# Optimization experiments

Measured on AMD Instinct MI355X. Metric: run time of the kernel, lower is better.

Reference implementation:

```python
import jax, jax.numpy as jnp
import numpy as np

B, T, C = 2, 2048, 2048
H, KVH, HD = 16, 4, 128  # heads, kv heads, head_dim
G = H // KVH             # GQA group size
THETA = 10000.0


def _rope_cos_sin(t, hd, dtype):
    inv_freq = 1.0 / (THETA ** (jnp.arange(0, hd, 2, dtype=jnp.float32) / hd))
    pos = jnp.arange(t, dtype=jnp.float32)
    freqs = pos[:, None] * inv_freq[None, :]          # [T, hd/2]
    emb = jnp.concatenate([freqs, freqs], axis=-1)    # [T, hd]
    return jnp.cos(emb).astype(dtype), jnp.sin(emb).astype(dtype)


def _rotate_half(x):
    x1, x2 = jnp.split(x, 2, axis=-1)
    return jnp.concatenate([-x2, x1], axis=-1)


def setup_inputs() -> dict:
    key = jax.random.key(0)
    ks = jax.random.split(key, 5)
    s_in = 1.0 / np.sqrt(C)
    return {
        "x": jax.random.normal(ks[0], (B, T, C), jnp.float32),
        "wq": jax.random.normal(ks[1], (C, H * HD), jnp.float32) * s_in,
        "bq": jnp.zeros((H * HD,), jnp.float32),
        "wk": jax.random.normal(ks[2], (C, KVH * HD), jnp.float32) * s_in,
        "bk": jnp.zeros((KVH * HD,), jnp.float32),
        "wv": jax.random.normal(ks[3], (C, KVH * HD), jnp.float32) * s_in,
        "bv": jnp.zeros((KVH * HD,), jnp.float32),
        "wo": jax.random.normal(ks[4], (H * HD, C), jnp.float32) * (1.0 / np.sqrt(H * HD)),
    }


def reference(x, wq, bq, wk, bk, wv, bv, wo):
    b, t, c = x.shape
    q = (x @ wq + bq).reshape(b, t, H, HD).transpose(0, 2, 1, 3)    # [B,H,T,hd]
    k = (x @ wk + bk).reshape(b, t, KVH, HD).transpose(0, 2, 1, 3)  # [B,KVH,T,hd]
    v = (x @ wv + bv).reshape(b, t, KVH, HD).transpose(0, 2, 1, 3)

    cos, sin = _rope_cos_sin(t, HD, x.dtype)  # [T,hd]
    q = q * cos + _rotate_half(q) * sin
    k = k * cos + _rotate_half(k) * sin

    # GQA: group query heads over kv heads
    qg = q.reshape(b, KVH, G, t, HD)
    scale = 1.0 / np.sqrt(HD)
    scores = jnp.einsum('bkgtd,bksd->bkgts', qg, k) * scale  # [B,KVH,G,T,T]
    causal = jnp.tril(jnp.ones((t, t), bool))
    scores = jnp.where(causal, scores, jnp.finfo(scores.dtype).min)
    attn = jax.nn.softmax(scores, axis=-1)
    out = jnp.einsum('bkgts,bksd->bkgtd', attn, v)            # [B,KVH,G,T,hd]
    out = out.reshape(b, H, t, HD).transpose(0, 2, 1, 3).reshape(b, t, H * HD)
    return out @ wo
```

## Files before the change

### kernel.cpp

```cpp
#include <hip/hip_runtime.h>
#include <hip/hip_bf16.h>
#include <math.h>

#define B_ 2
#define T_ 2048
#define C_ 2048
#define H_ 16
#define KVH_ 4
#define HD_ 128
#define G_ (H_ / KVH_)
#define MROWS (B_ * T_)
#define NQKV (H_ * HD_ + 2 * KVH_ * HD_)
#define KOFF (H_ * HD_)
#define VOFF (H_ * HD_ + KVH_ * HD_)
#define L2T (13.287712379549449f / 64.0f)

typedef __hip_bfloat16 bf16;
typedef short bf16x8 __attribute__((ext_vector_type(8)));
typedef short bf16x4 __attribute__((ext_vector_type(4)));
typedef float f32x4 __attribute__((ext_vector_type(4)));

__device__ __forceinline__ void gload_lds16(const void* g, void* l) {
  __builtin_amdgcn_global_load_lds(
      (const __attribute__((address_space(1))) unsigned int*)g,
      (__attribute__((address_space(3))) unsigned int*)l, 16, 0, 0);
}

static __device__ __forceinline__ f32x4 mfma32k(bf16x8 a, bf16x8 b, f32x4 c) {
  return __builtin_amdgcn_mfma_f32_16x16x32_bf16(a, b, c, 0, 0, 0);
}

static __device__ __forceinline__ short f2bf(float x) {
  unsigned u = __builtin_bit_cast(unsigned, x);
  u += 0x7FFFu + ((u >> 16) & 1u);
  return (short)(u >> 16);
}

static __device__ __forceinline__ float bfh2f(short h) {
  unsigned u = ((unsigned)(unsigned short)h) << 16;
  return __builtin_bit_cast(float, u);
}

static __device__ __forceinline__ float fexp2(float x) {
#if __has_builtin(__builtin_amdgcn_exp2f)
  return __builtin_amdgcn_exp2f(x);
#else
  return exp2f(x);
#endif
}

__global__ __launch_bounds__(256) void prep_kernel(
    const float* __restrict__ x, bf16* __restrict__ xb,
    const float* __restrict__ wq, const float* __restrict__ wk,
    const float* __restrict__ wv, bf16* __restrict__ wqkvT,
    const float* __restrict__ wo, bf16* __restrict__ woT,
    float2* __restrict__ tab) {
  __shared__ float t[32][33];
  int bid = blockIdx.x;
  if (bid < 8192) {
    const int i = (bid * 256 + threadIdx.x) * 4;
    float4 v = *(const float4*)(x + i);
    xb[i + 0] = __float2bfloat16(v.x);
    xb[i + 1] = __float2bfloat16(v.y);
    xb[i + 2] = __float2bfloat16(v.z);
    xb[i + 3] = __float2bfloat16(v.w);
    return;
  }
  bid -= 8192;
  if (bid < 6144) {
    const int tx = threadIdx.x & 31, ty = threadIdx.x >> 5;
    const int c0 = (bid % 96) * 32;
    const int r0 = (bid / 96) * 32;
    const float* src;
    int nn, ld;
    if (c0 < KOFF)      { src = wq; nn = c0;        ld = 2048; }
    else if (c0 < VOFF) { src = wk; nn = c0 - KOFF; ld = 512; }
    else                { src = wv; nn = c0 - VOFF; ld = 512; }
#pragma unroll
    for (int it = 0; it < 4; ++it)
      t[ty + 8 * it][tx] = src[(size_t)(r0 + ty + 8 * it) * ld + nn + tx];
    __syncthreads();
#pragma unroll
    for (int it = 0; it < 4; ++it)
      wqkvT[(size_t)(c0 + ty + 8 * it) * 2048 + r0 + tx] =
          __float2bfloat16(t[tx][ty + 8 * it]);
    return;
  }
  bid -= 6144;
  if (bid < 4096) {
    const int tx = threadIdx.x & 31, ty = threadIdx.x >> 5;
    const int c0 = (bid & 63) * 32;
    const int r0 = (bid >> 6) * 32;
#pragma unroll
    for (int it = 0; it < 4; ++it)
      t[ty + 8 * it][tx] = wo[(size_t)(r0 + ty + 8 * it) * 2048 + c0 + tx];
    __syncthreads();
#pragma unroll
    for (int it = 0; it < 4; ++it)
      woT[(size_t)(c0 + ty + 8 * it) * 2048 + r0 + tx] =
          __float2bfloat16(t[tx][ty + 8 * it]);
    return;
  }
  bid -= 4096;
  {
    const int idx = bid * 256 + threadIdx.x;
    const int tt = idx >> 6, i = idx & 63;
    const float invf = fexp2(-(float)i * L2T);
    float s, c;
    __sincosf((float)tt * invf, &s, &c);
    tab[idx] = make_float2(c, s);
  }
}

__global__ __launch_bounds__(256) void pack_kv(const bf16* __restrict__ qkv,
                                               bf16* __restrict__ kp,
                                               bf16* __restrict__ vp,
                                               const float2* __restrict__ tab) {
  const int pid = blockIdx.x;
  if (pid < 512) {
    const int tile = pid & 63;
    const int bk = pid >> 6;
    const int b = bk >> 2, kvh = bk & 3;
#pragma unroll
    for (int u = 0; u < 2; ++u) {
      const int t = threadIdx.x + u * 256;
      const int kc = t >> 6, L = t & 63;
      const int trow = tile * 32 + ((L >> 2) & 3) * 8 + (kc >> 2) * 4 + (L & 3);
      const bf16* src = qkv + (size_t)(b * T_ + trow) * NQKV +
                        KOFF + kvh * HD_ + (kc & 3) * 32 + (L >> 4) * 8;
      bf16x8 vs = *(const bf16x8*)src;
      bf16x8 vpair = *(const bf16x8*)(src + (((kc & 2) == 0) ? 64 : -64));
      const float2* tp = tab + trow * 64 + (kc & 1) * 32 + (L >> 4) * 8;
      bf16x8 outv;
#pragma unroll
      for (int jj = 0; jj < 8; ++jj) {
        const float2 cs = tp[jj];
        const float a = bfh2f(vs[jj]), p = bfh2f(vpair[jj]);
        outv[jj] = f2bf(((kc & 2) == 0) ? (a * cs.x - p * cs.y)
                                        : (a * cs.x + p * cs.y));
      }
      *(bf16x8*)(kp + ((size_t)(bk * 64 + tile) * 8 + kc) * 512 + L * 8) = outv;
    }
    return;
  }
  {
    const int pid2 = pid - 512;
    const int tile = pid2 & 63;
    const int bk = pid2 >> 6;
    const int b = bk >> 2, kvh = bk & 3;
#pragma unroll
    for (int u = 0; u < 2; ++u) {
      const int t = threadIdx.x + u * 256;
      const int ht = t >> 6, L = t & 63;
      const int colL = L & 15, quad = L >> 4;
      const bf16* base = qkv + (size_t)(b * T_ + tile * 32 + quad * 8) * NQKV +
                         VOFF + kvh * HD_ + ht * 16 + colL;
      bf16x8 v;
#pragma unroll
      for (int jj = 0; jj < 8; ++jj)
        v[jj] = *(const short*)(base + (size_t)jj * NQKV);
      *(bf16x8*)(vp + ((size_t)(bk * 64 + tile) * 8 + ht) * 512 + L * 8) = v;
    }
  }
}

template <bool BF16OUT>
__global__ __launch_bounds__(256, 2) void gemm_mfma64(
    const bf16* __restrict__ A, const bf16* __restrict__ Bt, void* __restrict__ Cout,
    const float* __restrict__ bq, const float* __restrict__ bk2,
    const float* __restrict__ bv2, int M, int N, int K) {
  __shared__ __align__(16) bf16 As[128 * 64];
  __shared__ __align__(16) bf16 Bs[128 * 64];
  const int tid = threadIdx.x;
  const int w = tid >> 6, lane = tid & 63;
  const int colL = lane & 15, quad = lane >> 4;
  const int wm = w & 1, wn = w >> 1;
  const int r0 = blockIdx.y * 128, c0 = blockIdx.x * 128;
  const int lrow = lane >> 3;
  const int lsl = ((lane & 7) ^ lrow) * 8;
  const int c7 = colL & 7;
  const int sq0 = (quad ^ c7) * 8;
  const int sq1 = ((4 + quad) ^ c7) * 8;

  f32x4 acc[4][4];
  const f32x4 zero = {0.f, 0.f, 0.f, 0.f};
#pragma unroll
  for (int mt = 0; mt < 4; ++mt)
#pragma unroll
    for (int nt = 0; nt < 4; ++nt) acc[mt][nt] = zero;

  const bf16* pa = A + (size_t)(r0 + lrow) * K + lsl;
  const bf16* pb = Bt + (size_t)(c0 + lrow) * K + lsl;

  for (int k0 = 0; k0 < K; k0 += 64) {
    __syncthreads();
#pragma unroll
    for (int it = 0; it < 4; ++it) {
      const int seg = it * 4 + w;
      gload_lds16(pa + (size_t)seg * 8 * K + k0, &As[seg * 8 * 64]);
      gload_lds16(pb + (size_t)seg * 8 * K + k0, &Bs[seg * 8 * 64]);
    }
    __syncthreads();
#pragma unroll
    for (int ks = 0; ks < 2; ++ks) {
      const int sq = ks ? sq1 : sq0;
      bf16x8 af[4], bfv[4];
#pragma unroll
      for (int mt = 0; mt < 4; ++mt)
        af[mt] = *(const bf16x8*)&As[(wm * 64 + mt * 16 + colL) * 64 + sq];
#pragma unroll
      for (int nt = 0; nt < 4; ++nt)
        bfv[nt] = *(const bf16x8*)&Bs[(wn * 64 + nt * 16 + colL) * 64 + sq];
#pragma unroll
      for (int mt = 0; mt < 4; ++mt)
#pragma unroll
        for (int nt = 0; nt < 4; ++nt)
          acc[mt][nt] = mfma32k(af[mt], bfv[nt], acc[mt][nt]);
    }
  }

#pragma unroll
  for (int nt = 0; nt < 4; ++nt) {
    const int c = c0 + wn * 64 + nt * 16 + colL;
    float bias = 0.f;
    if (bq) bias = (c < KOFF) ? bq[c] : (c < VOFF ? bk2[c - KOFF] : bv2[c - VOFF]);
#pragma unroll
    for (int mt = 0; mt < 4; ++mt) {
#pragma unroll
      for (int i = 0; i < 4; ++i) {
        const int r = r0 + wm * 64 + mt * 16 + quad * 4 + i;
        const float v = acc[mt][nt][i] + bias;
        if (BF16OUT)
          ((bf16*)Cout)[(size_t)r * N + c] = __float2bfloat16(v);
        else
          ((float*)Cout)[(size_t)r * N + c] = v;
      }
    }
  }
}

#define FA_SCL2 (0.08838834764831845f * 1.4426950408889634f)
#define FA_M2 16.0f

__global__ __launch_bounds__(256, 4) void flash_mfma8(
    const bf16* __restrict__ qkv, const bf16* __restrict__ kp,
    const bf16* __restrict__ vp, bf16* __restrict__ ao,
    const float2* __restrict__ tab) {
  __shared__ __align__(16) bf16 KS[3][4096];
  __shared__ __align__(16) bf16 VS[2][4096];

  const int id = blockIdx.x;
  const int bk = id & 7;
  const int u = id >> 3;
  const int av = u >> 5, vv = u & 31;
  const int jq = (av == 0) ? vv : (av == 1) ? (63 - vv)
               : (av == 2) ? (64 + vv) : (127 - vv);
  const int b = bk >> 2, kvh = bk & 3;
  const int w = threadIdx.x >> 6;
  const int h = (kvh << 2) | w;
  const int lane = threadIdx.x & 63;
  const int colL = lane & 15, quad = lane >> 4;
  const int myq0 = jq * 16;
  const int nkv = (jq >> 1) + 1;

  const bf16* kpt = kp + ((size_t)(bk * 64)) * 4096 + (w * 2) * 512 + lane * 8;
  const bf16* vpt = vp + ((size_t)(bk * 64)) * 4096 + (w * 2) * 512 + lane * 8;

  auto stageK = [&](int tile, int slot) {
    const bf16* s = kpt + (size_t)tile * 4096;
    bf16* d = &KS[slot][(w * 2) * 512];
    gload_lds16(s, d);
    gload_lds16(s + 512, d + 512);
  };
  auto stageV = [&](int tile, int slot) {
    const bf16* s = vpt + (size_t)tile * 4096;
    bf16* d = &VS[slot][(w * 2) * 512];
    gload_lds16(s, d);
    gload_lds16(s + 512, d + 512);
  };

  bf16x8 qf[4];
  {
    const bf16* qg = qkv + (size_t)(b * T_ + myq0) * NQKV + h * HD_;
    bf16x8 rq[4];
#pragma unroll
    for (int c = 0; c < 4; ++c)
      rq[c] = *(const bf16x8*)(qg + (size_t)colL * NQKV + c * 32 + quad * 8);
    const float2* tp = tab + (myq0 + colL) * 64 + quad * 8;
    float2 cs0[8], cs1[8];
#pragma unroll
    for (int jj = 0; jj < 8; ++jj) { cs0[jj] = tp[jj]; cs1[jj] = tp[32 + jj]; }
#pragma unroll
    for (int c = 0; c < 4; ++c) {
#pragma unroll
      for (int jj = 0; jj < 8; ++jj) {
        const float2 cs = (c & 1) ? cs1[jj] : cs0[jj];
        const float a = bfh2f(rq[c][jj]), p = bfh2f(rq[c ^ 2][jj]);
        qf[c][jj] = f2bf((c & 2) ? (a * cs.x + p * cs.y)
                                 : (a * cs.x - p * cs.y));
      }
    }
  }

  const f32x4 zero = {0.f, 0.f, 0.f, 0.f};
  auto qk = [&](const bf16* Kb, f32x4 (&s_)[2]) {
    s_[0] = zero; s_[1] = zero;
#pragma unroll
    for (int c = 0; c < 4; ++c) {
      bf16x8 kf0 = *(const bf16x8*)(Kb + c * 512 + lane * 8);
      bf16x8 kf1 = *(const bf16x8*)(Kb + (4 + c) * 512 + lane * 8);
      s_[0] = mfma32k(kf0, qf[c], s_[0]);
      s_[1] = mfma32k(kf1, qf[c], s_[1]);
    }
  };

  f32x4 o[8];
#pragma unroll
  for (int ht = 0; ht < 8; ++ht) o[ht] = zero;
  float l_ = 0.f;

  stageK(0, 0);
  if (nkv > 1) stageK(1, 1);
  if (nkv > 2) stageK(2, 2);
  stageV(0, 0);
  asm volatile("s_waitcnt vmcnt(0)\n\ts_barrier" ::: "memory");

  f32x4 sA[2], sB[2];
  qk(KS[0], sA);

  int kStage = 0, kNext = 1;
#pragma unroll 1
  for (int tt = 0; tt < nkv; ++tt) {
    const bool sv = (tt + 1 < nkv), sk = (tt + 3 < nkv);
    if (sv) stageV(tt + 1, (tt + 1) & 1);
    if (sk) stageK(tt + 3, kStage);

    if (sv) qk(KS[kNext], sB);

    bf16x4 pf[2];
    if (tt == nkv - 1) {
      const int qg = ((jq & 1) << 4) | colL;
#pragma unroll
      for (int kt = 0; kt < 2; ++kt) {
        const int kb = quad * 8 + kt * 4;
        float pv[4];
#pragma unroll
        for (int i = 0; i < 4; ++i) {
          float e = fexp2(fmaf(sA[kt][i], FA_SCL2, -FA_M2));
          pv[i] = (kb + i <= qg) ? e : 0.f;
        }
        l_ += (pv[0] + pv[1]) + (pv[2] + pv[3]);
        pf[kt] = (bf16x4){f2bf(pv[0]), f2bf(pv[1]), f2bf(pv[2]), f2bf(pv[3])};
      }
    } else {
#pragma unroll
      for (int kt = 0; kt < 2; ++kt) {
        float pv[4];
#pragma unroll
        for (int i = 0; i < 4; ++i)
          pv[i] = fexp2(fmaf(sA[kt][i], FA_SCL2, -FA_M2));
        l_ += (pv[0] + pv[1]) + (pv[2] + pv[3]);
        pf[kt] = (bf16x4){f2bf(pv[0]), f2bf(pv[1]), f2bf(pv[2]), f2bf(pv[3])};
      }
    }

    {
      const bf16* Vb = VS[tt & 1];
      const bf16x8 pcat = __builtin_shufflevector(pf[0], pf[1], 0, 1, 2, 3, 4, 5, 6, 7);
#pragma unroll
      for (int ht = 0; ht < 8; ++ht) {
        bf16x8 vf8 = *(const bf16x8*)(Vb + ht * 512 + lane * 8);
        o[ht] = mfma32k(vf8, pcat, o[ht]);
      }
    }

    if (sk) asm volatile("s_waitcnt vmcnt(2)\n\ts_barrier" ::: "memory");
    else    asm volatile("s_waitcnt vmcnt(0)\n\ts_barrier" ::: "memory");

    sA[0] = sB[0]; sA[1] = sB[1];
    kStage = (kStage == 2) ? 0 : kStage + 1;
    kNext  = (kNext == 2) ? 0 : kNext + 1;
  }

  {
    float lv = l_;
    lv += __shfl_xor(lv, 16);
    lv += __shfl_xor(lv, 32);
    const float rl = 1.f / lv;
    const size_t rbase = (size_t)(b * T_ + myq0 + colL) * (H_ * HD_) + h * HD_;
#pragma unroll
    for (int ht = 0; ht < 8; ++ht) {
      bf16x4 ov;
#pragma unroll
      for (int i = 0; i < 4; ++i) ov[i] = f2bf(o[ht][i] * rl);
      *(bf16x4*)(ao + rbase + ht * 16 + quad * 4) = ov;
    }
  }
}

extern "C" void kernel_launch(void* const* d_in, const int* in_sizes, int n_in,
                              void* d_out, int out_size, void* d_ws, size_t ws_size,
                              hipStream_t stream) {
  (void)in_sizes; (void)n_in; (void)out_size; (void)ws_size;
  const float* x  = (const float*)d_in[0];
  const float* wq = (const float*)d_in[1];
  const float* bq = (const float*)d_in[2];
  const float* wk = (const float*)d_in[3];
  const float* bk = (const float*)d_in[4];
  const float* wv = (const float*)d_in[5];
  const float* bv = (const float*)d_in[6];
  const float* wo = (const float*)d_in[7];
  float* out = (float*)d_out;

  char* ws = (char*)d_ws;
  bf16* xb    = (bf16*)ws;
  bf16* wqkvT = (bf16*)(ws + (16u << 20));
  bf16* woT   = (bf16*)(ws + (28u << 20));
  bf16* qkv   = (bf16*)(ws + (36u << 20));
  bf16* kp    = (bf16*)(ws + (60u << 20));
  bf16* vp    = (bf16*)(ws + (68u << 20));
  float2* tab = (float2*)(ws + (76u << 20));

  prep_kernel<<<dim3(18944), dim3(256), 0, stream>>>(
      x, xb, wq, wk, wv, wqkvT, wo, woT, tab);

  gemm_mfma64<true><<<dim3(NQKV / 128, MROWS / 128), dim3(256), 0, stream>>>(
      xb, wqkvT, qkv, bq, bk, bv, MROWS, NQKV, C_);

  pack_kv<<<dim3(1024), dim3(256), 0, stream>>>(qkv, kp, vp, tab);

  bf16* ao = xb;
  flash_mfma8<<<dim3(1024), dim3(256), 0, stream>>>(qkv, kp, vp, ao, tab);

  gemm_mfma64<false><<<dim3(C_ / 128, MROWS / 128), dim3(256), 0, stream>>>(
      ao, woT, out, nullptr, nullptr, nullptr, MROWS, C_, KOFF);
}
```

Measured before the change: 289.6 us.

## Fuse K/V rope and packing into QKV GEMM epilogue, simplify flash block order

Removes the separate pack_kv kernel. The QKV GEMM blocks that cover K and V columns now stage their tile in swizzled shared memory, apply RoPE to K and write the packed kp/vp layouts directly. This saves one kernel launch and one global read/write round trip of K/V. The flash attention block-to-query mapping is also changed from an interleaved scheme to a plain longest-first (reverse) order, which may change load balance.

Result: no change. 287.0 us (-0.9%).

```diff
diff --git a/kernel.cpp b/kernel.cpp
--- a/kernel.cpp
+++ b/kernel.cpp
@@ -112,65 +112,15 @@
   }
 }
 
-__global__ __launch_bounds__(256) void pack_kv(const bf16* __restrict__ qkv,
-                                               bf16* __restrict__ kp,
-                                               bf16* __restrict__ vp,
-                                               const float2* __restrict__ tab) {
-  const int pid = blockIdx.x;
-  if (pid < 512) {
-    const int tile = pid & 63;
-    const int bk = pid >> 6;
-    const int b = bk >> 2, kvh = bk & 3;
-#pragma unroll
-    for (int u = 0; u < 2; ++u) {
-      const int t = threadIdx.x + u * 256;
-      const int kc = t >> 6, L = t & 63;
-      const int trow = tile * 32 + ((L >> 2) & 3) * 8 + (kc >> 2) * 4 + (L & 3);
-      const bf16* src = qkv + (size_t)(b * T_ + trow) * NQKV +
-                        KOFF + kvh * HD_ + (kc & 3) * 32 + (L >> 4) * 8;
-      bf16x8 vs = *(const bf16x8*)src;
-      bf16x8 vpair = *(const bf16x8*)(src + (((kc & 2) == 0) ? 64 : -64));
-      const float2* tp = tab + trow * 64 + (kc & 1) * 32 + (L >> 4) * 8;
-      bf16x8 outv;
-#pragma unroll
-      for (int jj = 0; jj < 8; ++jj) {
-        const float2 cs = tp[jj];
-        const float a = bfh2f(vs[jj]), p = bfh2f(vpair[jj]);
-        outv[jj] = f2bf(((kc & 2) == 0) ? (a * cs.x - p * cs.y)
-                                        : (a * cs.x + p * cs.y));
-      }
-      *(bf16x8*)(kp + ((size_t)(bk * 64 + tile) * 8 + kc) * 512 + L * 8) = outv;
-    }
-    return;
-  }
-  {
-    const int pid2 = pid - 512;
-    const int tile = pid2 & 63;
-    const int bk = pid2 >> 6;
-    const int b = bk >> 2, kvh = bk & 3;
-#pragma unroll
-    for (int u = 0; u < 2; ++u) {
-      const int t = threadIdx.x + u * 256;
-      const int ht = t >> 6, L = t & 63;
-      const int colL = L & 15, quad = L >> 4;
-      const bf16* base = qkv + (size_t)(b * T_ + tile * 32 + quad * 8) * NQKV +
-                         VOFF + kvh * HD_ + ht * 16 + colL;
-      bf16x8 v;
-#pragma unroll
-      for (int jj = 0; jj < 8; ++jj)
-        v[jj] = *(const short*)(base + (size_t)jj * NQKV);
-      *(bf16x8*)(vp + ((size_t)(bk * 64 + tile) * 8 + ht) * 512 + L * 8) = v;
-    }
-  }
-}
-
-template <bool BF16OUT>
+template <bool BF16OUT, bool FUSE>
 __global__ __launch_bounds__(256, 2) void gemm_mfma64(
     const bf16* __restrict__ A, const bf16* __restrict__ Bt, void* __restrict__ Cout,
     const float* __restrict__ bq, const float* __restrict__ bk2,
-    const float* __restrict__ bv2, int M, int N, int K) {
-  __shared__ __align__(16) bf16 As[128 * 64];
-  __shared__ __align__(16) bf16 Bs[128 * 64];
+    const float* __restrict__ bv2, int M, int N, int K,
+    bf16* __restrict__ kp, bf16* __restrict__ vp, const float2* __restrict__ tab) {
+  __shared__ __align__(16) short SH[2 * 128 * 64];
+  short* As = SH;
+  short* Bs = SH + 128 * 64;
   const int tid = threadIdx.x;
   const int w = tid >> 6, lane = tid & 63;
   const int colL = lane & 15, quad = lane >> 4;
@@ -219,21 +169,80 @@
     }
   }
 
-#pragma unroll
-  for (int nt = 0; nt < 4; ++nt) {
-    const int c = c0 + wn * 64 + nt * 16 + colL;
-    float bias = 0.f;
-    if (bq) bias = (c < KOFF) ? bq[c] : (c < VOFF ? bk2[c - KOFF] : bv2[c - VOFF]);
-#pragma unroll
-    for (int mt = 0; mt < 4; ++mt) {
-#pragma unroll
-      for (int i = 0; i < 4; ++i) {
-        const int r = r0 + wm * 64 + mt * 16 + quad * 4 + i;
-        const float v = acc[mt][nt][i] + bias;
-        if (BF16OUT)
-          ((bf16*)Cout)[(size_t)r * N + c] = __float2bfloat16(v);
-        else
-          ((float*)Cout)[(size_t)r * N + c] = v;
+  if (!FUSE || c0 < KOFF) {
+#pragma unroll
+    for (int nt = 0; nt < 4; ++nt) {
+      const int c = c0 + wn * 64 + nt * 16 + colL;
+      float bias = 0.f;
+      if (bq) bias = (c < KOFF) ? bq[c] : (c < VOFF ? bk2[c - KOFF] : bv2[c - VOFF]);
+#pragma unroll
+      for (int mt = 0; mt < 4; ++mt) {
+#pragma unroll
+        for (int i = 0; i < 4; ++i) {
+          const int r = r0 + wm * 64 + mt * 16 + quad * 4 + i;
+          const float v = acc[mt][nt][i] + bias;
+          if (BF16OUT)
+            ((bf16*)Cout)[(size_t)r * N + c] = __float2bfloat16(v);
+          else
+            ((float*)Cout)[(size_t)r * N + c] = v;
+        }
+      }
+    }
+  } else {
+    __syncthreads();
+    const bool isK = (c0 < VOFF);
+#pragma unroll
+    for (int nt = 0; nt < 4; ++nt) {
+      const int c = c0 + wn * 64 + nt * 16 + colL;
+      const float bias = isK ? bk2[c - KOFF] : bv2[c - VOFF];
+      const int col = wn * 64 + nt * 16 + colL;
+#pragma unroll
+      for (int mt = 0; mt < 4; ++mt) {
+#pragma unroll
+        for (int i = 0; i < 4; ++i) {
+          const int row = wm * 64 + mt * 16 + quad * 4 + i;
+          SH[row * 128 + (col ^ ((row & 7) << 3))] = f2bf(acc[mt][nt][i] + bias);
+        }
+      }
+    }
+    __syncthreads();
+    const int b = r0 >> 11;
+    const int tbase = (r0 & 2047) >> 5;
+    const int kvh = (c0 - (isK ? KOFF : VOFF)) >> 7;
+    const int bkq = b * 4 + kvh;
+    if (isK) {
+#pragma unroll
+      for (int s = 0; s < 8; ++s) {
+        const int unit = s * 256 + tid;
+        const int L = unit & 63, kc = (unit >> 6) & 7, tile = unit >> 9;
+        const int trow = tile * 32 + ((L >> 2) & 3) * 8 + ((kc >> 2) << 2) + (L & 3);
+        const int d = (kc & 3) * 32 + ((L >> 4) << 3);
+        const int sx = (trow & 7) << 3;
+        bf16x8 lo = *(const bf16x8*)&SH[trow * 128 + (d ^ sx)];
+        bf16x8 hi = *(const bf16x8*)&SH[trow * 128 + ((d ^ 64) ^ sx)];
+        const int t_abs = (r0 + trow) & (T_ - 1);
+        const float2* tp = tab + t_abs * 64 + (d & 63);
+        bf16x8 outv;
+#pragma unroll
+        for (int j = 0; j < 8; ++j) {
+          const float2 cs = tp[j];
+          const float a = bfh2f(lo[j]), p = bfh2f(hi[j]);
+          outv[j] = f2bf((d < 64) ? (a * cs.x - p * cs.y) : (a * cs.x + p * cs.y));
+        }
+        *(bf16x8*)(kp + ((size_t)((bkq * 64 + tbase + tile) * 8 + kc)) * 512 + L * 8) = outv;
+      }
+    } else {
+#pragma unroll
+      for (int s = 0; s < 8; ++s) {
+        const int unit = s * 256 + tid;
+        const int L = unit & 63, ht = (unit >> 6) & 7, tile = unit >> 9;
+        const int rowb = tile * 32 + ((L >> 4) << 3);
+        const int colv = ht * 16 + (L & 15);
+        bf16x8 v;
+#pragma unroll
+        for (int j = 0; j < 8; ++j)
+          v[j] = SH[(rowb + j) * 128 + (colv ^ (((rowb + j) & 7) << 3))];
+        *(bf16x8*)(vp + ((size_t)((bkq * 64 + tbase + tile) * 8 + ht)) * 512 + L * 8) = v;
       }
     }
   }
@@ -252,9 +261,7 @@
   const int id = blockIdx.x;
   const int bk = id & 7;
   const int u = id >> 3;
-  const int av = u >> 5, vv = u & 31;
-  const int jq = (av == 0) ? vv : (av == 1) ? (63 - vv)
-               : (av == 2) ? (64 + vv) : (127 - vv);
+  const int jq = 127 - u;
   const int b = bk >> 2, kvh = bk & 3;
   const int w = threadIdx.x >> 6;
   const int h = (kvh << 2) | w;
@@ -424,14 +431,13 @@
   prep_kernel<<<dim3(18944), dim3(256), 0, stream>>>(
       x, xb, wq, wk, wv, wqkvT, wo, woT, tab);
 
-  gemm_mfma64<true><<<dim3(NQKV / 128, MROWS / 128), dim3(256), 0, stream>>>(
-      xb, wqkvT, qkv, bq, bk, bv, MROWS, NQKV, C_);
-
-  pack_kv<<<dim3(1024), dim3(256), 0, stream>>>(qkv, kp, vp, tab);
+  gemm_mfma64<true, true><<<dim3(NQKV / 128, MROWS / 128), dim3(256), 0, stream>>>(
+      xb, wqkvT, qkv, bq, bk, bv, MROWS, NQKV, C_, kp, vp, tab);
 
   bf16* ao = xb;
   flash_mfma8<<<dim3(1024), dim3(256), 0, stream>>>(qkv, kp, vp, ao, tab);
 
-  gemm_mfma64<false><<<dim3(C_ / 128, MROWS / 128), dim3(256), 0, stream>>>(
-      ao, woT, out, nullptr, nullptr, nullptr, MROWS, C_, KOFF);
-}
+  gemm_mfma64<false, false><<<dim3(C_ / 128, MROWS / 128), dim3(256), 0, stream>>>(
+      ao, woT, out, nullptr, nullptr, nullptr, MROWS, C_, KOFF,
+      nullptr, nullptr, nullptr);
+}
```
